# Optimization experiments

Measured on AMD Instinct MI355X. Metric: run time of the kernel, lower is better.

## Reference

```python
import jax, jax.numpy as jnp
import numpy as np
from jax import lax

DIM = 128
WINDOW = 5
K = 2 * WINDOW + 1
LAYER_GNN = 3
LAYER_CNN = 3
LAYER_OUT = 2
N_FP = 100000
N_WORD = 20000
N_ATOMS = 16384
N_WORDS = 16384


def setup_inputs() -> dict:
    key = jax.random.key(0)
    ks = jax.random.split(key, 16)
    s = 0.05  # small init scale to keep residual GNN stable
    adjacency = (jax.random.uniform(ks[1], (N_ATOMS, N_ATOMS)) < 0.002).astype(jnp.float32)
    return {
        "fingerprints": jax.random.randint(ks[0], (N_ATOMS,), 0, N_FP),
        "adjacency": adjacency,
        "words": jax.random.randint(ks[2], (N_WORDS,), 0, N_WORD),
        "embed_fp": jax.random.normal(ks[3], (N_FP, DIM)) * s,
        "embed_word": jax.random.normal(ks[4], (N_WORD, DIM)) * s,
        # shared weights (ModuleList([m]*k) in torch shares one module)
        "Wg": jax.random.normal(ks[5], (DIM, DIM)) * s,
        "bg": jnp.zeros((DIM,)),
        "conv_k": jax.random.normal(ks[6], (1, 1, K, K)) * s,  # OIHW
        "conv_b": jnp.zeros((1,)),
        "Wa": jax.random.normal(ks[7], (DIM, DIM)) * s,
        "ba": jnp.zeros((DIM,)),
        "Wo": jax.random.normal(ks[8], (2 * DIM, 2 * DIM)) * s,
        "bo": jnp.zeros((2 * DIM,)),
        "Wi": jax.random.normal(ks[9], (2, 2 * DIM)) * s,
        "bi": jnp.zeros((2,)),
    }


def reference(fingerprints, adjacency, words, embed_fp, embed_word,
              Wg, bg, conv_k, conv_b, Wa, ba, Wo, bo, Wi, bi):
    # --- GNN over molecule graph (shared weights across layers) ---
    xs = embed_fp[fingerprints]  # [N_ATOMS, DIM]
    for _ in range(LAYER_GNN):
        hs = jax.nn.relu(xs @ Wg.T + bg)
        xs = xs + adjacency @ hs
    compound = jnp.mean(xs, axis=0, keepdims=True)  # [1, DIM]

    # --- CNN over protein word embeddings (shared conv) ---
    ws = embed_word[words]  # [N_WORDS, DIM]
    img = ws[None, None]  # [1,1,L,D] NCHW
    for _ in range(LAYER_CNN):
        img = lax.conv_general_dilated(
            img, conv_k, window_strides=(1, 1),
            padding=[(WINDOW, WINDOW), (WINDOW, WINDOW)],
            dimension_numbers=("NCHW", "OIHW", "NCHW"))
        img = jax.nn.relu(img + conv_b[None, :, None, None])
    xs_p = img[0, 0]  # [N_WORDS, DIM]

    # --- attention pooling of protein conditioned on compound ---
    h = jax.nn.relu(compound @ Wa.T + ba)      # [1, DIM]
    hs = jax.nn.relu(xs_p @ Wa.T + ba)         # [L, DIM]
    weights = jnp.tanh(h @ hs.T)               # [1, L]
    ys = weights.T * hs                        # [L, DIM]
    protein = jnp.mean(ys, axis=0, keepdims=True)  # [1, DIM]

    # --- output MLP (shared weights across layers) ---
    cat = jnp.concatenate([compound, protein], axis=1)  # [1, 2*DIM]
    for _ in range(LAYER_OUT):
        cat = jax.nn.relu(cat @ Wo.T + bo)
    interaction = cat @ Wi.T + bi  # [1, 2]
    return interaction
```

## Files before the change

kernel.cpp:

```cpp
#include <hip/hip_runtime.h>
#include <hip/hip_bf16.h>
#include <math.h>

#define DIM 128
#define NATOMS 16384
#define NWORDS 16384
#define CAP 128
#define KW 11

__device__ __forceinline__ float bfu2f(unsigned short u) {
    unsigned int x = ((unsigned int)u) << 16;
    return __uint_as_float(x);
}

__global__ void k_zero256(float* __restrict__ p) {
    p[threadIdx.x] = 0.f;
}

__global__ void k_transpose128(const float* __restrict__ W, float* __restrict__ Wt) {
    int idx = blockIdx.x * 256 + threadIdx.x;
    int n = idx >> 7, k = idx & 127;
    Wt[k * DIM + n] = W[n * DIM + k];
}

__global__ void k_gather(const int* __restrict__ ids, const float* __restrict__ table,
                         float* __restrict__ out) {
    int idx = blockIdx.x * 256 + threadIdx.x;
    int i = idx >> 7, d = idx & 127;
    out[idx] = table[(size_t)ids[i] * DIM + d];
}

__global__ void k_csr(const float* __restrict__ adj, unsigned short* __restrict__ cols,
                      int* __restrict__ rowcnt) {
    __shared__ int cnt;
    int row = blockIdx.x;
    if (threadIdx.x == 0) cnt = 0;
    __syncthreads();
    const float4* rp = (const float4*)(adj + (size_t)row * NATOMS);
    unsigned short* rc = cols + (size_t)row * CAP;
    #pragma unroll
    for (int it = 0; it < NATOMS / 4 / 256; ++it) {
        int vi = it * 256 + threadIdx.x;
        float4 v = rp[vi];
        int j0 = vi * 4;
        if (v.x != 0.f) { int p = atomicAdd(&cnt, 1); if (p < CAP) rc[p] = (unsigned short)(j0); }
        if (v.y != 0.f) { int p = atomicAdd(&cnt, 1); if (p < CAP) rc[p] = (unsigned short)(j0 + 1); }
        if (v.z != 0.f) { int p = atomicAdd(&cnt, 1); if (p < CAP) rc[p] = (unsigned short)(j0 + 2); }
        if (v.w != 0.f) { int p = atomicAdd(&cnt, 1); if (p < CAP) rc[p] = (unsigned short)(j0 + 3); }
    }
    __syncthreads();
    if (threadIdx.x == 0) rowcnt[row] = min(cnt, CAP);
}

__global__ void k_gemm_relu(const float* __restrict__ A, const float* __restrict__ Wt,
                            const float* __restrict__ bias, __hip_bfloat16* __restrict__ out) {
    __shared__ float a_s[8][DIM];
    int row0 = blockIdx.x * 8;
    int t = threadIdx.x;
    #pragma unroll
    for (int p = 0; p < 4; ++p) {
        int e = p * 256 + t;
        a_s[e >> 7][e & 127] = A[(size_t)(row0 + (e >> 7)) * DIM + (e & 127)];
    }
    __syncthreads();
    int n = t & 127;
    int rh = (t >> 7) * 4;
    float acc0 = 0.f, acc1 = 0.f, acc2 = 0.f, acc3 = 0.f;
    #pragma unroll 4
    for (int k = 0; k < DIM; ++k) {
        float w = Wt[k * DIM + n];
        acc0 += a_s[rh + 0][k] * w;
        acc1 += a_s[rh + 1][k] * w;
        acc2 += a_s[rh + 2][k] * w;
        acc3 += a_s[rh + 3][k] * w;
    }
    float b = bias[n];
    out[(size_t)(row0 + rh + 0) * DIM + n] = __float2bfloat16(fmaxf(acc0 + b, 0.f));
    out[(size_t)(row0 + rh + 1) * DIM + n] = __float2bfloat16(fmaxf(acc1 + b, 0.f));
    out[(size_t)(row0 + rh + 2) * DIM + n] = __float2bfloat16(fmaxf(acc2 + b, 0.f));
    out[(size_t)(row0 + rh + 3) * DIM + n] = __float2bfloat16(fmaxf(acc3 + b, 0.f));
}

__global__ void k_spmm(float* __restrict__ xs, const unsigned short* __restrict__ cols,
                       const int* __restrict__ rowcnt, const __hip_bfloat16* __restrict__ hs) {
    int row = blockIdx.x;
    int d = threadIdx.x;
    int cnt = rowcnt[row];
    const unsigned short* rc = cols + (size_t)row * CAP;
    const unsigned short* hu = (const unsigned short*)hs;
    float acc = 0.f;
    int e = 0;
    for (; e + 4 <= cnt; e += 4) {
        int j0 = rc[e], j1 = rc[e + 1], j2 = rc[e + 2], j3 = rc[e + 3];
        acc += bfu2f(hu[(size_t)j0 * DIM + d]);
        acc += bfu2f(hu[(size_t)j1 * DIM + d]);
        acc += bfu2f(hu[(size_t)j2 * DIM + d]);
        acc += bfu2f(hu[(size_t)j3 * DIM + d]);
    }
    for (; e < cnt; ++e) acc += bfu2f(hu[(size_t)rc[e] * DIM + d]);
    xs[(size_t)row * DIM + d] += acc;
}

__global__ void k_colsum(const float* __restrict__ xs, float* __restrict__ sum) {
    int d = threadIdx.x;
    int r0 = blockIdx.x * 128;
    float acc = 0.f;
    for (int r = 0; r < 128; ++r) acc += xs[(size_t)(r0 + r) * DIM + d];
    atomicAdd(&sum[d], acc);
}

#define TY 16
__global__ void k_conv(const float* __restrict__ in, const float* __restrict__ kw,
                       const float* __restrict__ kb, float* __restrict__ out) {
    __shared__ float buf[TY + 10][144];
    __shared__ float kk[121];
    int t = threadIdx.x;
    if (t < 121) kk[t] = kw[t];
    int y0 = blockIdx.x * TY;
    for (int rr = 0; rr < TY + 10; ++rr) {
        int r = y0 - 5 + rr;
        bool rok = (r >= 0 && r < NWORDS);
        {
            int xi = t - 5;
            buf[rr][t] = (rok && xi >= 0) ? in[(size_t)r * DIM + xi] : 0.f;
        }
        if (t < 10) {
            int xi = t + 123;
            buf[rr][t + 128] = (rok && xi < DIM) ? in[(size_t)r * DIM + xi] : 0.f;
        }
    }
    __syncthreads();
    float acc[TY];
    #pragma unroll
    for (int o = 0; o < TY; ++o) acc[o] = 0.f;
    float bias = kb[0];
    #pragma unroll
    for (int rr = 0; rr < TY + 10; ++rr) {
        float v[KW];
        #pragma unroll
        for (int dx = 0; dx < KW; ++dx) v[dx] = buf[rr][t + dx];
        #pragma unroll
        for (int dy = 0; dy < KW; ++dy) {
            int o = rr - dy;
            if (o >= 0 && o < TY) {
                float s = 0.f;
                #pragma unroll
                for (int dx = 0; dx < KW; ++dx) s += v[dx] * kk[dy * KW + dx];
                acc[o] += s;
            }
        }
    }
    #pragma unroll
    for (int o = 0; o < TY; ++o)
        out[(size_t)(y0 + o) * DIM + t] = fmaxf(acc[o] + bias, 0.f);
}

__global__ void k_hvec(const float* __restrict__ csum, const float* __restrict__ Wa,
                       const float* __restrict__ ba, float* __restrict__ h) {
    __shared__ float c[DIM];
    int t = threadIdx.x;
    c[t] = csum[t] * (1.f / (float)NATOMS);
    __syncthreads();
    float acc = ba[t];
    for (int k = 0; k < DIM; ++k) acc += c[k] * Wa[t * DIM + k];
    h[t] = fmaxf(acc, 0.f);
}

__global__ void k_attnpool(const __hip_bfloat16* __restrict__ hs, const float* __restrict__ h,
                           float* __restrict__ psum) {
    __shared__ float ls[DIM];
    int t = threadIdx.x;
    if (t < DIM) ls[t] = 0.f;
    __syncthreads();
    int lane = t & 63;
    int wave = blockIdx.x * 4 + (t >> 6);
    int d0 = lane * 2;
    float h0 = h[d0], h1 = h[d0 + 1];
    const unsigned short* hu = (const unsigned short*)hs;
    float a0 = 0.f, a1 = 0.f;
    for (int r = wave; r < NWORDS; r += 512) {
        ushort2 uv = *(const ushort2*)(hu + (size_t)r * DIM + d0);
        float v0 = bfu2f(uv.x), v1 = bfu2f(uv.y);
        float p = h0 * v0 + h1 * v1;
        #pragma unroll
        for (int m = 32; m >= 1; m >>= 1) p += __shfl_xor(p, m, 64);
        float w = tanhf(p);
        a0 += w * v0;
        a1 += w * v1;
    }
    atomicAdd(&ls[d0], a0);
    atomicAdd(&ls[d0 + 1], a1);
    __syncthreads();
    if (t < DIM) atomicAdd(&psum[t], ls[t]);
}

__global__ void k_mlp(const float* __restrict__ csum, const float* __restrict__ psum,
                      const float* __restrict__ Wo, const float* __restrict__ bo,
                      const float* __restrict__ Wi, const float* __restrict__ bi,
                      float* __restrict__ out) {
    __shared__ float cat[256];
    __shared__ float nxt[256];
    int t = threadIdx.x;
    cat[t] = (t < DIM ? csum[t] : psum[t - DIM]) * (1.f / 16384.f);
    __syncthreads();
    for (int L = 0; L < 2; ++L) {
        float acc = bo[t];
        for (int k = 0; k < 256; ++k) acc += cat[k] * Wo[t * 256 + k];
        nxt[t] = fmaxf(acc, 0.f);
        __syncthreads();
        cat[t] = nxt[t];
        __syncthreads();
    }
    if (t < 2) {
        float acc = bi[t];
        for (int k = 0; k < 256; ++k) acc += cat[k] * Wi[t * 256 + k];
        out[t] = acc;
    }
}

extern "C" void kernel_launch(void* const* d_in, const int* in_sizes, int n_in,
                              void* d_out, int out_size, void* d_ws, size_t ws_size,
                              hipStream_t stream) {
    const int*   fingerprints = (const int*)  d_in[0];
    const float* adj          = (const float*)d_in[1];
    const int*   words        = (const int*)  d_in[2];
    const float* embed_fp     = (const float*)d_in[3];
    const float* embed_word   = (const float*)d_in[4];
    const float* Wg           = (const float*)d_in[5];
    const float* bg           = (const float*)d_in[6];
    const float* convk        = (const float*)d_in[7];
    const float* convb        = (const float*)d_in[8];
    const float* Wa           = (const float*)d_in[9];
    const float* ba           = (const float*)d_in[10];
    const float* Wo           = (const float*)d_in[11];
    const float* bo           = (const float*)d_in[12];
    const float* Wi           = (const float*)d_in[13];
    const float* bi           = (const float*)d_in[14];
    float* out = (float*)d_out;

    char* ws = (char*)d_ws;
    float*            xs     = (float*)           (ws + 0);
    __hip_bfloat16*   hsb    = (__hip_bfloat16*)  (ws + 8388608);
    unsigned short*   cols   = (unsigned short*)  (ws + 12582912);
    int*              rowcnt = (int*)             (ws + 16777216);
    float*            imgA   = (float*)           (ws + 16842752);
    float*            imgB   = (float*)           (ws + 25231360);
    __hip_bfloat16*   hsp    = (__hip_bfloat16*)  (ws + 33619968);
    float*            Wtg    = (float*)           (ws + 37814272);
    float*            Wta    = (float*)           (ws + 37879808);
    float*            csum   = (float*)           (ws + 37945344);
    float*            psum   = (float*)           (ws + 37945856);
    float*            hvec   = (float*)           (ws + 37946368);

    k_zero256<<<1, 256, 0, stream>>>(csum);
    k_transpose128<<<64, 256, 0, stream>>>(Wg, Wtg);
    k_transpose128<<<64, 256, 0, stream>>>(Wa, Wta);
    k_gather<<<8192, 256, 0, stream>>>(fingerprints, embed_fp, xs);
    k_csr<<<16384, 256, 0, stream>>>(adj, cols, rowcnt);

    for (int l = 0; l < 3; ++l) {
        k_gemm_relu<<<2048, 256, 0, stream>>>(xs, Wtg, bg, hsb);
        k_spmm<<<16384, 128, 0, stream>>>(xs, cols, rowcnt, hsb);
    }
    k_colsum<<<128, 128, 0, stream>>>(xs, csum);

    k_gather<<<8192, 256, 0, stream>>>(words, embed_word, imgA);
    k_conv<<<1024, 128, 0, stream>>>(imgA, convk, convb, imgB);
    k_conv<<<1024, 128, 0, stream>>>(imgB, convk, convb, imgA);
    k_conv<<<1024, 128, 0, stream>>>(imgA, convk, convb, imgB);

    k_gemm_relu<<<2048, 256, 0, stream>>>(imgB, Wta, ba, hsp);
    k_hvec<<<1, 128, 0, stream>>>(csum, Wa, ba, hvec);
    k_attnpool<<<128, 256, 0, stream>>>(hsp, hvec, psum);
    k_mlp<<<1, 256, 0, stream>>>(csum, psum, Wo, bo, Wi, bi, out);
}
```

Baseline: 2.038 ms.

## Use bf16 MFMA for dense GEMMs and fuse weight prep kernels

Replaces the scalar fp32 GEMM+ReLU with a bf16 MFMA 16x16x32 kernel where each wave computes 16 rows across all 128 columns, converting activations and weights to bf16. Weight preparation (bf16 casts, Wo transpose, zeroing) is merged into one prep kernel, and the output MLP now reads a transposed Wo for coalesced access. This cuts GEMM compute time and launch count but rounds GEMM inputs to bf16, adding precision loss.

```diff
diff --git a/kernel.cpp b/kernel.cpp
--- a/kernel.cpp
+++ b/kernel.cpp
@@ -8,19 +8,37 @@
 #define CAP 128
 #define KW 11
 
+typedef float f32x4 __attribute__((ext_vector_type(4)));
+typedef __bf16 bf16x8 __attribute__((ext_vector_type(8)));
+typedef unsigned short us8 __attribute__((ext_vector_type(8)));
+
 __device__ __forceinline__ float bfu2f(unsigned short u) {
     unsigned int x = ((unsigned int)u) << 16;
     return __uint_as_float(x);
 }
-
-__global__ void k_zero256(float* __restrict__ p) {
-    p[threadIdx.x] = 0.f;
-}
-
-__global__ void k_transpose128(const float* __restrict__ W, float* __restrict__ Wt) {
+__device__ __forceinline__ unsigned short f2bf(float f) {
+    unsigned int x = __float_as_uint(f);
+    unsigned int r = (x + 0x7fffu + ((x >> 16) & 1u)) >> 16;
+    return (unsigned short)r;
+}
+
+__global__ void k_prep(const float* __restrict__ Wg, const float* __restrict__ Wa,
+                       const float* __restrict__ Wo,
+                       unsigned short* __restrict__ Wgbf, unsigned short* __restrict__ Wabf,
+                       float* __restrict__ WoT, float* __restrict__ zeros) {
     int idx = blockIdx.x * 256 + threadIdx.x;
-    int n = idx >> 7, k = idx & 127;
-    Wt[k * DIM + n] = W[n * DIM + k];
+    if (idx < 16384) {
+        Wgbf[idx] = f2bf(Wg[idx]);
+    } else if (idx < 32768) {
+        int e = idx - 16384;
+        Wabf[e] = f2bf(Wa[e]);
+    } else if (idx < 98304) {
+        int e = idx - 32768;
+        int r = e >> 8, c = e & 255;
+        WoT[c * 256 + r] = Wo[e];
+    } else if (idx < 98560) {
+        zeros[idx - 98304] = 0.f;
+    }
 }
 
 __global__ void k_gather(const int* __restrict__ ids, const float* __restrict__ table,
@@ -52,33 +70,46 @@
     if (threadIdx.x == 0) rowcnt[row] = min(cnt, CAP);
 }
 
-__global__ void k_gemm_relu(const float* __restrict__ A, const float* __restrict__ Wt,
-                            const float* __restrict__ bias, __hip_bfloat16* __restrict__ out) {
-    __shared__ float a_s[8][DIM];
-    int row0 = blockIdx.x * 8;
-    int t = threadIdx.x;
-    #pragma unroll
-    for (int p = 0; p < 4; ++p) {
-        int e = p * 256 + t;
-        a_s[e >> 7][e & 127] = A[(size_t)(row0 + (e >> 7)) * DIM + (e & 127)];
-    }
-    __syncthreads();
-    int n = t & 127;
-    int rh = (t >> 7) * 4;
-    float acc0 = 0.f, acc1 = 0.f, acc2 = 0.f, acc3 = 0.f;
-    #pragma unroll 4
-    for (int k = 0; k < DIM; ++k) {
-        float w = Wt[k * DIM + n];
-        acc0 += a_s[rh + 0][k] * w;
-        acc1 += a_s[rh + 1][k] * w;
-        acc2 += a_s[rh + 2][k] * w;
-        acc3 += a_s[rh + 3][k] * w;
-    }
-    float b = bias[n];
-    out[(size_t)(row0 + rh + 0) * DIM + n] = __float2bfloat16(fmaxf(acc0 + b, 0.f));
-    out[(size_t)(row0 + rh + 1) * DIM + n] = __float2bfloat16(fmaxf(acc1 + b, 0.f));
-    out[(size_t)(row0 + rh + 2) * DIM + n] = __float2bfloat16(fmaxf(acc2 + b, 0.f));
-    out[(size_t)(row0 + rh + 3) * DIM + n] = __float2bfloat16(fmaxf(acc3 + b, 0.f));
+__global__ __launch_bounds__(256) void k_gemm_mfma(const float* __restrict__ A,
+                                                   const unsigned short* __restrict__ Wbf,
+                                                   const float* __restrict__ bias,
+                                                   __hip_bfloat16* __restrict__ out) {
+    int t = threadIdx.x;
+    int wave = t >> 6, lane = t & 63;
+    int m16 = lane & 15, kgrp = lane >> 4;
+    int r0 = blockIdx.x * 64 + wave * 16;
+    const float* arow = A + (size_t)(r0 + m16) * DIM;
+
+    bf16x8 afrag[4];
+    #pragma unroll
+    for (int kb = 0; kb < 4; ++kb) {
+        const float4* p = (const float4*)(arow + kb * 32 + kgrp * 8);
+        float4 lo = p[0], hi = p[1];
+        us8 u;
+        u[0] = f2bf(lo.x); u[1] = f2bf(lo.y); u[2] = f2bf(lo.z); u[3] = f2bf(lo.w);
+        u[4] = f2bf(hi.x); u[5] = f2bf(hi.y); u[6] = f2bf(hi.z); u[7] = f2bf(hi.w);
+        union { us8 u; bf16x8 b; } cv; cv.u = u;
+        afrag[kb] = cv.b;
+    }
+
+    unsigned short* outp = (unsigned short*)out;
+    for (int nb = 0; nb < 8; ++nb) {
+        int col = nb * 16 + m16;
+        const unsigned short* brow = Wbf + (size_t)col * DIM;
+        f32x4 acc = {0.f, 0.f, 0.f, 0.f};
+        #pragma unroll
+        for (int kb = 0; kb < 4; ++kb) {
+            union { us8 u; bf16x8 b; } cv;
+            cv.u = *(const us8*)(brow + kb * 32 + kgrp * 8);
+            acc = __builtin_amdgcn_mfma_f32_16x16x32_bf16(afrag[kb], cv.b, acc, 0, 0, 0);
+        }
+        float b = bias[col];
+        #pragma unroll
+        for (int q = 0; q < 4; ++q) {
+            int row = r0 + kgrp * 4 + q;
+            outp[(size_t)row * DIM + col] = f2bf(fmaxf(acc[q] + b, 0.f));
+        }
+    }
 }
 
 __global__ void k_spmm(float* __restrict__ xs, const unsigned short* __restrict__ cols,
@@ -195,7 +226,7 @@
 }
 
 __global__ void k_mlp(const float* __restrict__ csum, const float* __restrict__ psum,
-                      const float* __restrict__ Wo, const float* __restrict__ bo,
+                      const float* __restrict__ WoT, const float* __restrict__ bo,
                       const float* __restrict__ Wi, const float* __restrict__ bi,
                       float* __restrict__ out) {
     __shared__ float cat[256];
@@ -205,7 +236,7 @@
     __syncthreads();
     for (int L = 0; L < 2; ++L) {
         float acc = bo[t];
-        for (int k = 0; k < 256; ++k) acc += cat[k] * Wo[t * 256 + k];
+        for (int k = 0; k < 256; ++k) acc += cat[k] * WoT[k * 256 + t];
         nxt[t] = fmaxf(acc, 0.f);
         __syncthreads();
         cat[t] = nxt[t];
@@ -246,20 +277,19 @@
     float*            imgA   = (float*)           (ws + 16842752);
     float*            imgB   = (float*)           (ws + 25231360);
     __hip_bfloat16*   hsp    = (__hip_bfloat16*)  (ws + 33619968);
-    float*            Wtg    = (float*)           (ws + 37814272);
-    float*            Wta    = (float*)           (ws + 37879808);
-    float*            csum   = (float*)           (ws + 37945344);
-    float*            psum   = (float*)           (ws + 37945856);
-    float*            hvec   = (float*)           (ws + 37946368);
-
-    k_zero256<<<1, 256, 0, stream>>>(csum);
-    k_transpose128<<<64, 256, 0, stream>>>(Wg, Wtg);
-    k_transpose128<<<64, 256, 0, stream>>>(Wa, Wta);
+    unsigned short*   Wgbf   = (unsigned short*)  (ws + 37814272);
+    unsigned short*   Wabf   = (unsigned short*)  (ws + 37847040);
+    float*            WoT    = (float*)           (ws + 37879808);
+    float*            csum   = (float*)           (ws + 38141952);
+    float*            psum   = (float*)           (ws + 38142464);
+    float*            hvec   = (float*)           (ws + 38142976);
+
+    k_prep<<<385, 256, 0, stream>>>(Wg, Wa, Wo, Wgbf, Wabf, WoT, csum);
     k_gather<<<8192, 256, 0, stream>>>(fingerprints, embed_fp, xs);
     k_csr<<<16384, 256, 0, stream>>>(adj, cols, rowcnt);
 
     for (int l = 0; l < 3; ++l) {
-        k_gemm_relu<<<2048, 256, 0, stream>>>(xs, Wtg, bg, hsb);
+        k_gemm_mfma<<<256, 256, 0, stream>>>(xs, Wgbf, bg, hsb);
         k_spmm<<<16384, 128, 0, stream>>>(xs, cols, rowcnt, hsb);
     }
     k_colsum<<<128, 128, 0, stream>>>(xs, csum);
@@ -269,8 +299,8 @@
     k_conv<<<1024, 128, 0, stream>>>(imgB, convk, convb, imgA);
     k_conv<<<1024, 128, 0, stream>>>(imgA, convk, convb, imgB);
 
-    k_gemm_relu<<<2048, 256, 0, stream>>>(imgB, Wta, ba, hsp);
+    k_gemm_mfma<<<256, 256, 0, stream>>>(imgB, Wabf, ba, hsp);
     k_hvec<<<1, 128, 0, stream>>>(csum, Wa, ba, hvec);
     k_attnpool<<<128, 256, 0, stream>>>(hsp, hvec, psum);
-    k_mlp<<<1, 256, 0, stream>>>(csum, psum, Wo, bo, Wi, bi, out);
-}
+    k_mlp<<<1, 256, 0, stream>>>(csum, psum, WoT, bo, Wi, bi, out);
+}
```

After: 1.970 ms. -3.4%, faster.
